# Kernel optimization log

Hardware: AMD Instinct MI355X
Metric: run time of the kernel (lower is better)

Reference implementation:

```python
import jax, jax.numpy as jnp
import numpy as np

B, L, H = 1, 2048, 2048          # batch, seq_len, hidden_size
E, N, K, R = 4096, 16, 4, 128    # intermediate, ssm_state, conv_kernel, dt_rank


def setup_inputs() -> dict:
    key = jax.random.key(0)
    ks = jax.random.split(key, 8)
    s = 0.02
    inp = {
        "hidden_states": jax.random.normal(ks[0], (B, L, H), jnp.float32),
        "in_proj_w": jax.random.normal(ks[1], (2 * E, H), jnp.float32) * s,
        "conv_w": jax.random.normal(ks[2], (E, 1, K), jnp.float32) * s,
        "conv_b": jax.random.normal(ks[3], (E,), jnp.float32) * s,
        "x_proj_w": jax.random.normal(ks[4], (R + 2 * N, E), jnp.float32) * s,
        "dt_proj_w": jax.random.normal(ks[5], (E, R), jnp.float32) * s,
        "dt_proj_b": jax.random.normal(ks[6], (E,), jnp.float32) * s,
        "A_log": jnp.broadcast_to(jnp.log(jnp.arange(1, N + 1, dtype=jnp.float32))[None, :], (E, N)).copy(),
        "D": jnp.ones((E,), jnp.float32),
        "out_proj_w": jax.random.normal(ks[7], (H, E), jnp.float32) * s,
    }
    return inp


def _mamba_mixer(hidden_states, in_proj_w, conv_w, conv_b, x_proj_w,
                 dt_proj_w, dt_proj_b, A_log, D, out_proj_w):
    # in_proj -> [B, L, 2E], split into hidden / gate
    proj = jnp.einsum('blh,eh->ble', hidden_states, in_proj_w)
    h, gate = jnp.split(proj, 2, axis=-1)            # each [B, L, E]

    # depthwise causal conv1d over time, padding K-1 on the left
    h_c = h.transpose(0, 2, 1)                       # [B, E, L]
    h_c = jax.lax.conv_general_dilated(
        h_c, conv_w, window_strides=(1,), padding=[(K - 1, 0)],
        feature_group_count=E, dimension_numbers=('NCH', 'OIH', 'NCH'))
    h_c = h_c + conv_b[None, :, None]
    h = jax.nn.silu(h_c).transpose(0, 2, 1)          # [B, L, E]

    # x_proj -> dt, B, C (input-dependent SSM params)
    ssm = jnp.einsum('ble,pe->blp', h, x_proj_w)     # [B, L, R+2N]
    dt, Bp, Cp = jnp.split(ssm, [R, R + N], axis=-1)
    dt = jax.nn.softplus(jnp.einsum('blr,er->ble', dt, dt_proj_w) + dt_proj_b)  # [B,L,E]

    A = -jnp.exp(A_log)                              # [E, N]
    dA = jnp.exp(dt[..., None] * A)                  # [B, L, E, N]
    dBu = (dt * h)[..., None] * Bp[:, :, None, :]    # [B, L, E, N]

    # selective scan: s_t = dA_t * s_{t-1} + dBu_t
    def step(s, xs):
        dA_t, dBu_t = xs
        s = s * dA_t + dBu_t
        return s, s

    s0 = jnp.zeros((h.shape[0], E, N), h.dtype)
    _, states = jax.lax.scan(step, s0, (dA.transpose(1, 0, 2, 3), dBu.transpose(1, 0, 2, 3)))
    # states: [L, B, E, N]
    y = jnp.einsum('lben,bln->ble', states, Cp)      # [B, L, E]
    y = y + h * D                                    # skip via D
    y = y * jax.nn.silu(gate)                        # gated output
    return jnp.einsum('ble,he->blh', y, out_proj_w)  # [B, L, H]


def reference(hidden_states, in_proj_w, conv_w, conv_b, x_proj_w,
              dt_proj_w, dt_proj_b, A_log, D, out_proj_w):
    return _mamba_mixer(hidden_states, in_proj_w, conv_w, conv_b, x_proj_w,
                        dt_proj_w, dt_proj_b, A_log, D, out_proj_w)
```

## Files before the change

### kernel.cpp

```cpp
#include <hip/hip_runtime.h>

#define LL 2048
#define HH 2048
#define EE 4096
#define NS 16
#define RR 128
#define CT 32
#define NC (LL / CT)
#define BM 128
#define BN 128
#define BK 64

typedef __bf16 bf16x8 __attribute__((ext_vector_type(8)));
typedef float f32x4 __attribute__((ext_vector_type(4)));

__device__ __forceinline__ unsigned short f2bf(float f) {
  union { float f; unsigned int u; } v; v.f = f;
  unsigned int r = v.u + 0x7fffu + ((v.u >> 16) & 1u);
  return (unsigned short)(r >> 16);
}

__device__ __forceinline__ float bf2f(unsigned short u) {
  union { unsigned int i; float f; } v;
  v.i = ((unsigned int)u) << 16;
  return v.f;
}

__device__ __forceinline__ float softplus_fast(float x) {
  if (x > 20.0f) return x;
  float e = __builtin_amdgcn_exp2f(1.44269504f * x);
  return 0.69314718f * __builtin_amdgcn_logf(1.0f + e);
}

__device__ __forceinline__ void async_cp16(const unsigned short* g,
                                           unsigned short* l) {
  __builtin_amdgcn_global_load_lds(
      (const __attribute__((address_space(1))) unsigned int*)g,
      (__attribute__((address_space(3))) unsigned int*)l, 16, 0, 0);
}

__global__ void cast_bf16_k(const float* __restrict__ in,
                            unsigned short* __restrict__ out, int n4) {
  int i = blockIdx.x * blockDim.x + threadIdx.x;
  if (i >= n4) return;
  float4 v = reinterpret_cast<const float4*>(in)[i];
  ushort4 o;
  o.x = f2bf(v.x); o.y = f2bf(v.y); o.z = f2bf(v.z); o.w = f2bf(v.w);
  reinterpret_cast<ushort4*>(out)[i] = o;
}

__global__ void zero_k(float* __restrict__ p, int n4) {
  int i = blockIdx.x * blockDim.x + threadIdx.x;
  if (i >= n4) return;
  float4 z; z.x = z.y = z.z = z.w = 0.0f;
  reinterpret_cast<float4*>(p)[i] = z;
}

template <int EPI>
__global__ __launch_bounds__(512, 2) void gemm256(
    const unsigned short* __restrict__ A,
    const unsigned short* __restrict__ B,
    float* __restrict__ C,
    int M, int N, int K, int tilesM, int splitk,
    float* __restrict__ auxF, unsigned short* __restrict__ auxB) {
  __shared__ __align__(16) unsigned short As[2][16384];
  __shared__ __align__(16) unsigned short Bs[2][16384];

  int bid = blockIdx.x;
  int tnInner = bid & 7;
  int rest = bid >> 3;
  int tm = rest % tilesM;
  int tn = (rest / tilesM) * 8 + tnInner;

  int Kslice = K / splitk;
  int k_begin = blockIdx.y * Kslice;
  int NT = Kslice / 64;

  int tid = threadIdx.x;
  int lane = tid & 63;
  int wave = tid >> 6;
  int wm = wave >> 2;
  int wn = wave & 3;
  int m16 = lane & 15, quad = lane >> 4;

  const unsigned short* Ab = A + (size_t)tm * 256 * K;
  const unsigned short* Bb = B + (size_t)tn * 256 * K;

  int rowS = tid >> 3;
  int gcbS = (tid & 7) ^ (rowS & 7);
  int ldsWB = (tid & ~63) * 8;

  int sw = m16 & 7;
  int coff0 = (quad ^ sw) << 3;
  int coff1 = ((4 + quad) ^ sw) << 3;
  int aoff = (wm * 128 + m16) * 64;
  int boff = (wn * 64 + m16) * 64;

  f32x4 acc[8][4];
#pragma unroll
  for (int i = 0; i < 8; ++i)
#pragma unroll
    for (int j = 0; j < 4; ++j)
#pragma unroll
      for (int t = 0; t < 4; ++t) acc[i][j][t] = 0.0f;

  auto stageA = [&](int bufb, int t, int h) {
    int kt = k_begin + t * 64;
    unsigned short* dst = &As[bufb][0];
#pragma unroll
    for (int c = 2 * h; c < 2 * h + 2; ++c)
      async_cp16(Ab + (size_t)(c * 64 + rowS) * K + kt + gcbS * 8,
                 dst + c * 4096 + ldsWB);
  };
  auto stageB = [&](int bufb, int t, int h) {
    int kt = k_begin + t * 64;
    unsigned short* dst = &Bs[bufb][0];
#pragma unroll
    for (int c = 2 * h; c < 2 * h + 2; ++c)
      async_cp16(Bb + (size_t)(c * 64 + rowS) * K + kt + gcbS * 8,
                 dst + c * 4096 + ldsWB);
  };

  stageA(0, 0, 0); stageA(0, 0, 1);
  stageB(0, 0, 0); stageB(0, 0, 1);
  stageB(1, 1, 0); stageB(1, 1, 1);
  stageA(1, 1, 0);
  asm volatile("s_waitcnt vmcnt(6)" ::: "memory");
  __builtin_amdgcn_s_barrier();

  bf16x8 a[4][2], b0[2][2], b1[2][2];

  for (int t0 = 0; t0 < NT; t0 += 2) {
    int t1 = t0 + 1;
    bool notLast = (t0 + 2 < NT);
    unsigned short* A0 = &As[0][0];
    unsigned short* B0 = &Bs[0][0];
    unsigned short* A1 = &As[1][0];
    unsigned short* B1 = &Bs[1][0];

#pragma unroll
    for (int i = 0; i < 4; ++i) {
      a[i][0] = *reinterpret_cast<const bf16x8*>(&A0[aoff + i * 1024 + coff0]);
      a[i][1] = *reinterpret_cast<const bf16x8*>(&A0[aoff + i * 1024 + coff1]);
    }
#pragma unroll
    for (int j = 0; j < 2; ++j) {
      b0[j][0] = *reinterpret_cast<const bf16x8*>(&B0[boff + j * 1024 + coff0]);
      b0[j][1] = *reinterpret_cast<const bf16x8*>(&B0[boff + j * 1024 + coff1]);
    }
    stageA(1, t1, 1);
    __builtin_amdgcn_s_barrier();
    asm volatile("s_waitcnt lgkmcnt(0)" ::: "memory");
    __builtin_amdgcn_sched_barrier(0);
    __builtin_amdgcn_s_setprio(1);
#pragma unroll
    for (int kk = 0; kk < 2; ++kk)
#pragma unroll
      for (int i = 0; i < 4; ++i)
#pragma unroll
        for (int j = 0; j < 2; ++j)
          acc[i][j] = __builtin_amdgcn_mfma_f32_16x16x32_bf16(
              a[i][kk], b0[j][kk], acc[i][j], 0, 0, 0);
    __builtin_amdgcn_s_setprio(0);
    __builtin_amdgcn_s_barrier();

#pragma unroll
    for (int j = 0; j < 2; ++j) {
      b1[j][0] = *reinterpret_cast<const bf16x8*>(&B0[boff + (2 + j) * 1024 + coff0]);
      b1[j][1] = *reinterpret_cast<const bf16x8*>(&B0[boff + (2 + j) * 1024 + coff1]);
    }
    __builtin_amdgcn_s_barrier();
    asm volatile("s_waitcnt lgkmcnt(0)" ::: "memory");
    __builtin_amdgcn_sched_barrier(0);
    __builtin_amdgcn_s_setprio(1);
#pragma unroll
    for (int kk = 0; kk < 2; ++kk)
#pragma unroll
      for (int i = 0; i < 4; ++i)
#pragma unroll
        for (int j = 0; j < 2; ++j)
          acc[i][2 + j] = __builtin_amdgcn_mfma_f32_16x16x32_bf16(
              a[i][kk], b1[j][kk], acc[i][2 + j], 0, 0, 0);
    __builtin_amdgcn_s_setprio(0);
    __builtin_amdgcn_s_barrier();

#pragma unroll
    for (int i = 0; i < 4; ++i) {
      a[i][0] = *reinterpret_cast<const bf16x8*>(&A0[aoff + (4 + i) * 1024 + coff0]);
      a[i][1] = *reinterpret_cast<const bf16x8*>(&A0[aoff + (4 + i) * 1024 + coff1]);
    }
    if (notLast) stageB(0, t0 + 2, 0);
    __builtin_amdgcn_s_barrier();
    asm volatile("s_waitcnt lgkmcnt(0)" ::: "memory");
    __builtin_amdgcn_sched_barrier(0);
    __builtin_amdgcn_s_setprio(1);
#pragma unroll
    for (int kk = 0; kk < 2; ++kk)
#pragma unroll
      for (int i = 0; i < 4; ++i)
#pragma unroll
        for (int j = 0; j < 2; ++j)
          acc[4 + i][2 + j] = __builtin_amdgcn_mfma_f32_16x16x32_bf16(
              a[i][kk], b1[j][kk], acc[4 + i][2 + j], 0, 0, 0);
    __builtin_amdgcn_s_setprio(0);
    __builtin_amdgcn_s_barrier();

    if (notLast) stageB(0, t0 + 2, 1);
    __builtin_amdgcn_s_setprio(1);
#pragma unroll
    for (int kk = 0; kk < 2; ++kk)
#pragma unroll
      for (int i = 0; i < 4; ++i)
#pragma unroll
        for (int j = 0; j < 2; ++j)
          acc[4 + i][j] = __builtin_amdgcn_mfma_f32_16x16x32_bf16(
              a[i][kk], b0[j][kk], acc[4 + i][j], 0, 0, 0);
    __builtin_amdgcn_s_setprio(0);
    if (notLast) {
      asm volatile("s_waitcnt vmcnt(4)" ::: "memory");
    } else {
      asm volatile("s_waitcnt vmcnt(0)" ::: "memory");
    }
    __builtin_amdgcn_s_barrier();

#pragma unroll
    for (int i = 0; i < 4; ++i) {
      a[i][0] = *reinterpret_cast<const bf16x8*>(&A1[aoff + i * 1024 + coff0]);
      a[i][1] = *reinterpret_cast<const bf16x8*>(&A1[aoff + i * 1024 + coff1]);
    }
#pragma unroll
    for (int j = 0; j < 2; ++j) {
      b0[j][0] = *reinterpret_cast<const bf16x8*>(&B1[boff + j * 1024 + coff0]);
      b0[j][1] = *reinterpret_cast<const bf16x8*>(&B1[boff + j * 1024 + coff1]);
    }
    if (notLast) stageA(0, t0 + 2, 0);
    __builtin_amdgcn_s_barrier();
    asm volatile("s_waitcnt lgkmcnt(0)" ::: "memory");
    __builtin_amdgcn_sched_barrier(0);
    __builtin_amdgcn_s_setprio(1);
#pragma unroll
    for (int kk = 0; kk < 2; ++kk)
#pragma unroll
      for (int i = 0; i < 4; ++i)
#pragma unroll
        for (int j = 0; j < 2; ++j)
          acc[i][j] = __builtin_amdgcn_mfma_f32_16x16x32_bf16(
              a[i][kk], b0[j][kk], acc[i][j], 0, 0, 0);
    __builtin_amdgcn_s_setprio(0);
    __builtin_amdgcn_s_barrier();

#pragma unroll
    for (int j = 0; j < 2; ++j) {
      b1[j][0] = *reinterpret_cast<const bf16x8*>(&B1[boff + (2 + j) * 1024 + coff0]);
      b1[j][1] = *reinterpret_cast<const bf16x8*>(&B1[boff + (2 + j) * 1024 + coff1]);
    }
    if (notLast) stageA(0, t0 + 2, 1);
    __builtin_amdgcn_s_barrier();
    asm volatile("s_waitcnt lgkmcnt(0)" ::: "memory");
    __builtin_amdgcn_sched_barrier(0);
    __builtin_amdgcn_s_setprio(1);
#pragma unroll
    for (int kk = 0; kk < 2; ++kk)
#pragma unroll
      for (int i = 0; i < 4; ++i)
#pragma unroll
        for (int j = 0; j < 2; ++j)
          acc[i][2 + j] = __builtin_amdgcn_mfma_f32_16x16x32_bf16(
              a[i][kk], b1[j][kk], acc[i][2 + j], 0, 0, 0);
    __builtin_amdgcn_s_setprio(0);
    __builtin_amdgcn_s_barrier();

#pragma unroll
    for (int i = 0; i < 4; ++i) {
      a[i][0] = *reinterpret_cast<const bf16x8*>(&A1[aoff + (4 + i) * 1024 + coff0]);
      a[i][1] = *reinterpret_cast<const bf16x8*>(&A1[aoff + (4 + i) * 1024 + coff1]);
    }
    if (notLast) stageB(1, t1 + 2, 0);
    __builtin_amdgcn_s_barrier();
    asm volatile("s_waitcnt lgkmcnt(0)" ::: "memory");
    __builtin_amdgcn_sched_barrier(0);
    __builtin_amdgcn_s_setprio(1);
#pragma unroll
    for (int kk = 0; kk < 2; ++kk)
#pragma unroll
      for (int i = 0; i < 4; ++i)
#pragma unroll
        for (int j = 0; j < 2; ++j)
          acc[4 + i][2 + j] = __builtin_amdgcn_mfma_f32_16x16x32_bf16(
              a[i][kk], b1[j][kk], acc[4 + i][2 + j], 0, 0, 0);
    __builtin_amdgcn_s_setprio(0);
    __builtin_amdgcn_s_barrier();

    if (notLast) { stageB(1, t1 + 2, 1); stageA(1, t1 + 2, 0); }
    __builtin_amdgcn_s_setprio(1);
#pragma unroll
    for (int kk = 0; kk < 2; ++kk)
#pragma unroll
      for (int i = 0; i < 4; ++i)
#pragma unroll
        for (int j = 0; j < 2; ++j)
          acc[4 + i][j] = __builtin_amdgcn_mfma_f32_16x16x32_bf16(
              a[i][kk], b0[j][kk], acc[4 + i][j], 0, 0, 0);
    __builtin_amdgcn_s_setprio(0);
    if (notLast) {
      asm volatile("s_waitcnt vmcnt(6)" ::: "memory");
    }
    __builtin_amdgcn_s_barrier();
  }

  int rowB = tm * 256 + wm * 128;
  int colB = tn * 256 + wn * 64;
  if constexpr (EPI == 1) {
#pragma unroll
    for (int mi = 0; mi < 8; ++mi)
#pragma unroll
      for (int nj = 0; nj < 4; ++nj) {
        int col = colB + nj * 16 + m16;
        int row0 = rowB + mi * 16 + quad * 4;
#pragma unroll
        for (int t4 = 0; t4 < 4; ++t4)
          atomicAdd(&C[(size_t)(row0 + t4) * N + col], acc[mi][nj][t4]);
      }
  } else {
    if (colB < EE) {
#pragma unroll
      for (int mi = 0; mi < 8; ++mi)
#pragma unroll
        for (int nj = 0; nj < 4; ++nj) {
          int col = colB + nj * 16 + m16;
          int row0 = rowB + mi * 16 + quad * 4;
#pragma unroll
          for (int t4 = 0; t4 < 4; ++t4)
            auxF[(size_t)(row0 + t4) * EE + col] = acc[mi][nj][t4];
        }
    } else {
#pragma unroll
      for (int mi = 0; mi < 8; ++mi)
#pragma unroll
        for (int nj = 0; nj < 4; ++nj) {
          int cg = colB + nj * 16 + m16 - EE;
          int row0 = rowB + mi * 16 + quad * 4;
#pragma unroll
          for (int t4 = 0; t4 < 4; ++t4) {
            float v = acc[mi][nj][t4];
            float s = v / (1.0f + __expf(-v));
            auxB[(size_t)(row0 + t4) * EE + cg] = f2bf(s);
          }
        }
    }
  }
}

template <int EPI>
__global__ __launch_bounds__(256) void gemm_lds_t(
    const unsigned short* __restrict__ A,
    const unsigned short* __restrict__ B,
    float* __restrict__ C,
    int M, int N, int K, int tilesM, int splitk,
    const float* __restrict__ bias, float* __restrict__ auxF,
    unsigned short* __restrict__ auxB) {
  __shared__ __align__(16) unsigned short As[BM * BK];
  __shared__ __align__(16) unsigned short Bs[BN * BK];

  int bid = blockIdx.x;
  int tnInner = bid & 7;
  int rest = bid >> 3;
  int tm = rest % tilesM;
  int tnOuter = rest / tilesM;
  int tn = tnOuter * 8 + tnInner;

  int Kslice = K / splitk;
  int k_begin = blockIdx.y * Kslice;
  int k_end = k_begin + Kslice;

  int tid = threadIdx.x;
  int lane = tid & 63;
  int wave = tid >> 6;
  int wm = wave & 1, wn = wave >> 1;
  int m16 = lane & 15, quad = lane >> 4;

  const unsigned short* Ab = A + (size_t)tm * BM * K;
  const unsigned short* Bb = B + (size_t)tn * BN * K;

  int srow[4], sgcb[4];
#pragma unroll
  for (int it = 0; it < 4; ++it) {
    int blk = it * 256 + tid;
    srow[it] = blk >> 3;
    sgcb[it] = (blk & 7) ^ (srow[it] & 7);
  }
  int ldsbase = (tid & ~63) * 8;

  f32x4 acc[4][4];
#pragma unroll
  for (int i = 0; i < 4; ++i)
#pragma unroll
    for (int j = 0; j < 4; ++j)
#pragma unroll
      for (int t = 0; t < 4; ++t) acc[i][j][t] = 0.0f;

  for (int k0 = k_begin; k0 < k_end; k0 += BK) {
    __syncthreads();
#pragma unroll
    for (int it = 0; it < 4; ++it)
      async_cp16(Ab + (size_t)srow[it] * K + k0 + sgcb[it] * 8,
                 &As[it * 2048 + ldsbase]);
#pragma unroll
    for (int it = 0; it < 4; ++it)
      async_cp16(Bb + (size_t)srow[it] * K + k0 + sgcb[it] * 8,
                 &Bs[it * 2048 + ldsbase]);
    __syncthreads();
#pragma unroll
    for (int kk = 0; kk < 2; ++kk) {
      bf16x8 a[4], b[4];
#pragma unroll
      for (int i = 0; i < 4; ++i) {
        int rr = wm * 64 + i * 16 + m16;
        int cb = (kk << 2) + quad;
        a[i] = *reinterpret_cast<const bf16x8*>(
            &As[rr * BK + ((cb ^ (rr & 7)) << 3)]);
      }
#pragma unroll
      for (int j = 0; j < 4; ++j) {
        int rr = wn * 64 + j * 16 + m16;
        int cb = (kk << 2) + quad;
        b[j] = *reinterpret_cast<const bf16x8*>(
            &Bs[rr * BK + ((cb ^ (rr & 7)) << 3)]);
      }
#pragma unroll
      for (int i = 0; i < 4; ++i)
#pragma unroll
        for (int j = 0; j < 4; ++j)
          acc[i][j] =
              __builtin_amdgcn_mfma_f32_16x16x32_bf16(a[i], b[j], acc[i][j], 0, 0, 0);
    }
  }

  int rowB = tm * BM + wm * 64;
  int colB = tn * BN + wn * 64;
  if constexpr (EPI == 1) {
#pragma unroll
    for (int i = 0; i < 4; ++i)
#pragma unroll
      for (int j = 0; j < 4; ++j) {
        int col = colB + j * 16 + m16;
        int row0 = rowB + i * 16 + quad * 4;
#pragma unroll
        for (int t = 0; t < 4; ++t)
          atomicAdd(&C[(size_t)(row0 + t) * N + col], acc[i][j][t]);
      }
  } else {
#pragma unroll
    for (int i = 0; i < 4; ++i)
#pragma unroll
      for (int j = 0; j < 4; ++j) {
        int col = colB + j * 16 + m16;
        float bv = bias[col];
        int row0 = rowB + i * 16 + quad * 4;
#pragma unroll
        for (int t = 0; t < 4; ++t) {
          float x = acc[i][j][t] + bv;
          auxB[(size_t)(row0 + t) * EE + col] = f2bf(softplus_fast(x));
        }
      }
  }
}

__global__ __launch_bounds__(256) void gemm_bt(
    const unsigned short* __restrict__ A,
    const unsigned short* __restrict__ B,
    float* __restrict__ C,
    int M, int N, int K, int tilesN, int splitk) {
  int bid = blockIdx.x;
  int groupSize = 8 * tilesN;
  int g = bid / groupSize, r = bid % groupSize;
  int tm = g * 8 + (r & 7);
  int tn = r >> 3;

  int Kslice = K / splitk;
  int k_begin = blockIdx.y * Kslice;
  int k_end = k_begin + Kslice;

  int tid = threadIdx.x;
  int wave = tid >> 6, lane = tid & 63;
  int wm = wave & 1, wn = wave >> 1;
  int m16 = lane & 15, quad = lane >> 4;
  int rowBase = tm * 64 + wm * 32;
  int colBase = tn * 128 + wn * 64;

  const unsigned short* a0p = A + (size_t)(rowBase + m16) * K + quad * 8;
  const unsigned short* a1p = A + (size_t)(rowBase + 16 + m16) * K + quad * 8;
  const unsigned short* bp[4];
  bool bok[4];
#pragma unroll
  for (int j = 0; j < 4; ++j) {
    int col = colBase + j * 16 + m16;
    bok[j] = (col < N);
    bp[j] = B + (size_t)(bok[j] ? col : 0) * K + quad * 8;
  }

  f32x4 acc[2][4];
#pragma unroll
  for (int i = 0; i < 2; ++i)
#pragma unroll
    for (int j = 0; j < 4; ++j)
#pragma unroll
      for (int t = 0; t < 4; ++t) acc[i][j][t] = 0.0f;

  bf16x8 zero8;
#pragma unroll
  for (int t = 0; t < 8; ++t) zero8[t] = (__bf16)0.0f;

  for (int k = k_begin; k < k_end; k += 32) {
    bf16x8 a0 = *reinterpret_cast<const bf16x8*>(a0p + k);
    bf16x8 a1 = *reinterpret_cast<const bf16x8*>(a1p + k);
    bf16x8 b[4];
#pragma unroll
    for (int j = 0; j < 4; ++j)
      b[j] = bok[j] ? *reinterpret_cast<const bf16x8*>(bp[j] + k) : zero8;
#pragma unroll
    for (int j = 0; j < 4; ++j) {
      acc[0][j] = __builtin_amdgcn_mfma_f32_16x16x32_bf16(a0, b[j], acc[0][j], 0, 0, 0);
      acc[1][j] = __builtin_amdgcn_mfma_f32_16x16x32_bf16(a1, b[j], acc[1][j], 0, 0, 0);
    }
  }

#pragma unroll
  for (int i = 0; i < 2; ++i)
#pragma unroll
    for (int j = 0; j < 4; ++j) {
      int col = colBase + j * 16 + m16;
      if (col >= N) continue;
      int row0 = rowBase + i * 16 + quad * 4;
      if (splitk == 1) {
#pragma unroll
        for (int t = 0; t < 4; ++t)
          C[(size_t)(row0 + t) * N + col] = acc[i][j][t];
      } else {
#pragma unroll
        for (int t = 0; t < 4; ++t)
          atomicAdd(&C[(size_t)(row0 + t) * N + col], acc[i][j][t]);
      }
    }
}

__global__ __launch_bounds__(256) void conv_silu_k(
    const float* __restrict__ projh, const float* __restrict__ cw,
    const float* __restrict__ cb, unsigned short* __restrict__ hb) {
  int e = blockIdx.x * 256 + threadIdx.x;
  int l0 = blockIdx.y * 16;
  float w0 = cw[e * 4 + 0], w1 = cw[e * 4 + 1];
  float w2 = cw[e * 4 + 2], w3 = cw[e * 4 + 3];
  float bias = cb[e];
  float xm3 = (l0 >= 3) ? projh[(size_t)(l0 - 3) * EE + e] : 0.0f;
  float xm2 = (l0 >= 2) ? projh[(size_t)(l0 - 2) * EE + e] : 0.0f;
  float xm1 = (l0 >= 1) ? projh[(size_t)(l0 - 1) * EE + e] : 0.0f;
#pragma unroll
  for (int t = 0; t < 16; ++t) {
    int l = l0 + t;
    float x0 = projh[(size_t)l * EE + e];
    float acc = bias + w0 * xm3 + w1 * xm2 + w2 * xm1 + w3 * x0;
    float s = acc / (1.0f + __expf(-acc));
    hb[(size_t)l * EE + e] = f2bf(s);
    xm3 = xm2; xm2 = xm1; xm1 = x0;
  }
}

__global__ void dtcast_k(const float* __restrict__ ssm,
                         unsigned short* __restrict__ dtin, int n) {
  int i = blockIdx.x * blockDim.x + threadIdx.x;
  if (i >= n) return;
  int l = i >> 7, r = i & 127;
  dtin[i] = f2bf(ssm[l * 160 + r]);
}

__global__ __launch_bounds__(256) void scan_partA(
    const unsigned short* __restrict__ dtb, const unsigned short* __restrict__ hb,
    const float* __restrict__ ssm, const float* __restrict__ A_log,
    float* __restrict__ P, float* __restrict__ S) {
  int e = blockIdx.y * 256 + threadIdx.x;
  int c = blockIdx.x;
  float Aa[16];
#pragma unroll
  for (int q = 0; q < 4; ++q) {
    float4 a = reinterpret_cast<const float4*>(&A_log[(size_t)e * NS])[q];
    Aa[q * 4 + 0] = -__expf(a.x) * 1.44269504f;
    Aa[q * 4 + 1] = -__expf(a.y) * 1.44269504f;
    Aa[q * 4 + 2] = -__expf(a.z) * 1.44269504f;
    Aa[q * 4 + 3] = -__expf(a.w) * 1.44269504f;
  }
  float s[16], p[16];
#pragma unroll
  for (int n = 0; n < 16; ++n) { s[n] = 0.0f; p[n] = 1.0f; }
  int l0 = c * CT;
#pragma unroll 2
  for (int t = 0; t < CT; ++t) {
    int l = l0 + t;
    size_t o = (size_t)l * EE + e;
    float dtv = bf2f(dtb[o]);
    float hv = bf2f(hb[o]);
    float Bv[16];
#pragma unroll
    for (int q = 0; q < 4; ++q)
      *reinterpret_cast<float4*>(&Bv[q * 4]) =
          reinterpret_cast<const float4*>(&ssm[(size_t)l * 160 + 128])[q];
    float z = dtv * hv;
#pragma unroll
    for (int n = 0; n < 16; ++n) {
      float dA = __builtin_amdgcn_exp2f(dtv * Aa[n]);
      s[n] = s[n] * dA + z * Bv[n];
      p[n] *= dA;
    }
  }
  size_t base = ((size_t)c * EE + e) * NS;
#pragma unroll
  for (int q = 0; q < 4; ++q) {
    reinterpret_cast<float4*>(&P[base])[q] = *reinterpret_cast<float4*>(&p[q * 4]);
    reinterpret_cast<float4*>(&S[base])[q] = *reinterpret_cast<float4*>(&s[q * 4]);
  }
}

__global__ __launch_bounds__(256) void scan_chunkB(
    const float* __restrict__ P, float* __restrict__ S) {
  int gidx = blockIdx.x * 256 + threadIdx.x;
  float s = 0.0f;
  float pv = P[gidx], sv = S[gidx];
  for (int c = 0; c < NC; ++c) {
    float pn = 0.0f, sn = 0.0f;
    if (c + 1 < NC) {
      size_t i2 = (size_t)(c + 1) * (EE * NS) + gidx;
      pn = P[i2];
      sn = S[i2];
    }
    float s_next = s * pv + sv;
    S[(size_t)c * (EE * NS) + gidx] = s;
    s = s_next;
    pv = pn; sv = sn;
  }
}

__global__ __launch_bounds__(256) void scan_partC(
    const unsigned short* __restrict__ dtb, const unsigned short* __restrict__ hb,
    const float* __restrict__ ssm, const float* __restrict__ A_log,
    const float* __restrict__ Dp, const unsigned short* __restrict__ sg,
    const float* __restrict__ Sinit, unsigned short* __restrict__ yb) {
  int e = blockIdx.y * 256 + threadIdx.x;
  int c = blockIdx.x;
  float Aa[16];
#pragma unroll
  for (int q = 0; q < 4; ++q) {
    float4 a = reinterpret_cast<const float4*>(&A_log[(size_t)e * NS])[q];
    Aa[q * 4 + 0] = -__expf(a.x) * 1.44269504f;
    Aa[q * 4 + 1] = -__expf(a.y) * 1.44269504f;
    Aa[q * 4 + 2] = -__expf(a.z) * 1.44269504f;
    Aa[q * 4 + 3] = -__expf(a.w) * 1.44269504f;
  }
  float Dv = Dp[e];
  float s[16];
  size_t base = ((size_t)c * EE + e) * NS;
#pragma unroll
  for (int q = 0; q < 4; ++q)
    *reinterpret_cast<float4*>(&s[q * 4]) =
        reinterpret_cast<const float4*>(&Sinit[base])[q];
  int l0 = c * CT;
#pragma unroll 2
  for (int t = 0; t < CT; ++t) {
    int l = l0 + t;
    size_t o = (size_t)l * EE + e;
    float dtv = bf2f(dtb[o]);
    float hv = bf2f(hb[o]);
    float Bv[16], Cv[16];
#pragma unroll
    for (int q = 0; q < 4; ++q) {
      *reinterpret_cast<float4*>(&Bv[q * 4]) =
          reinterpret_cast<const float4*>(&ssm[(size_t)l * 160 + 128])[q];
      *reinterpret_cast<float4*>(&Cv[q * 4]) =
          reinterpret_cast<const float4*>(&ssm[(size_t)l * 160 + 144])[q];
    }
    float z = dtv * hv;
    float y = 0.0f;
#pragma unroll
    for (int n = 0; n < 16; ++n) {
      float dA = __builtin_amdgcn_exp2f(dtv * Aa[n]);
      s[n] = s[n] * dA + z * Bv[n];
      y += s[n] * Cv[n];
    }
    float gv = bf2f(sg[o]);
    float yv = (y + hv * Dv) * gv;
    yb[o] = f2bf(yv);
  }
}

extern "C" void kernel_launch(void* const* d_in, const int* in_sizes, int n_in,
                              void* d_out, int out_size, void* d_ws, size_t ws_size,
                              hipStream_t stream) {
  const float* hs   = (const float*)d_in[0];
  const float* w1   = (const float*)d_in[1];
  const float* cw   = (const float*)d_in[2];
  const float* cb   = (const float*)d_in[3];
  const float* xw   = (const float*)d_in[4];
  const float* dtw  = (const float*)d_in[5];
  const float* dtb  = (const float*)d_in[6];
  const float* Alog = (const float*)d_in[7];
  const float* Dp   = (const float*)d_in[8];
  const float* ow   = (const float*)d_in[9];
  float* out = (float*)d_out;

  char* ws = (char*)d_ws;
  size_t off = 0;
  auto alloc = [&](size_t b) {
    char* p = ws + off;
    off += (b + 255) & ~(size_t)255;
    return p;
  };
  float* projh = (float*)alloc((size_t)LL * EE * 4);
  unsigned short* sg  = (unsigned short*)alloc((size_t)LL * EE * 2);
  unsigned short* hb  = (unsigned short*)alloc((size_t)LL * EE * 2);
  unsigned short* dtb_buf = (unsigned short*)alloc((size_t)LL * EE * 2);
  unsigned short* w1b = (unsigned short*)alloc((size_t)2 * EE * HH * 2);
  unsigned short* hsb = (unsigned short*)alloc((size_t)LL * HH * 2);
  unsigned short* yb  = (unsigned short*)alloc((size_t)LL * EE * 2);
  unsigned short* owb = (unsigned short*)alloc((size_t)HH * EE * 2);
  unsigned short* xwb = (unsigned short*)alloc((size_t)160 * EE * 2);
  float* ssm = (float*)alloc((size_t)LL * 160 * 4);
  unsigned short* dtin = (unsigned short*)alloc((size_t)LL * RR * 2);
  unsigned short* dtwb = (unsigned short*)alloc((size_t)EE * RR * 2);
  float* Pbuf = (float*)alloc((size_t)NC * EE * NS * 4);
  float* Sbuf = (float*)alloc((size_t)NC * EE * NS * 4);

  auto cast = [&](const float* in, unsigned short* o, int nelem) {
    int n4 = nelem / 4;
    cast_bf16_k<<<(n4 + 255) / 256, 256, 0, stream>>>(in, o, n4);
  };
  cast(hs, hsb, LL * HH);
  cast(w1, w1b, 2 * EE * HH);
  cast(xw, xwb, 160 * EE);
  cast(dtw, dtwb, EE * RR);
  cast(ow, owb, HH * EE);
  zero_k<<<(LL * 160 / 4 + 255) / 256, 256, 0, stream>>>(ssm, LL * 160 / 4);
  zero_k<<<(LL * HH / 4 + 255) / 256, 256, 0, stream>>>(out, LL * HH / 4);

  {
    int tilesM = LL / 256;
    int tilesN = (2 * EE) / 256;
    gemm256<2><<<dim3(tilesM * tilesN, 1), 512, 0, stream>>>(
        hsb, w1b, nullptr, LL, 2 * EE, HH, tilesM, 1, projh, sg);
  }
  conv_silu_k<<<dim3(EE / 256, LL / 16), 256, 0, stream>>>(projh, cw, cb, hb);
  {
    int tilesN = (160 + 127) / 128, tilesM = LL / 64;
    gemm_bt<<<dim3(tilesM * tilesN, 8), 256, 0, stream>>>(
        hb, xwb, ssm, LL, 160, EE, tilesN, 8);
  }
  dtcast_k<<<(LL * RR + 255) / 256, 256, 0, stream>>>(ssm, dtin, LL * RR);
  {
    int tilesN = EE / BN, tilesM = LL / BM;
    gemm_lds_t<4><<<dim3(tilesM * tilesN, 1), 256, 0, stream>>>(
        dtin, dtwb, nullptr, LL, EE, RR, tilesM, 1, dtb, nullptr, dtb_buf);
  }
  scan_partA<<<dim3(NC, EE / 256), 256, 0, stream>>>(dtb_buf, hb, ssm, Alog,
                                                     Pbuf, Sbuf);
  scan_chunkB<<<EE * NS / 256, 256, 0, stream>>>(Pbuf, Sbuf);
  scan_partC<<<dim3(NC, EE / 256), 256, 0, stream>>>(dtb_buf, hb, ssm, Alog, Dp,
                                                     sg, Sbuf, yb);
  {
    int tilesN = HH / BN, tilesM = LL / BM;
    gemm_lds_t<1><<<dim3(tilesM * tilesN, 2), 256, 0, stream>>>(
        yb, owb, out, LL, HH, EE, tilesM, 2, nullptr, nullptr, nullptr);
  }
}
```

Measured before the change: 419.6 us.

## Fuse cast/zero launches into one prep kernel; use 256-tile GEMM for out_proj

The five bf16 cast launches and two zero-fill launches are merged into a single prep kernel that picks its source and destination by index range, cutting launch overhead. The output projection moves from the 128x128 LDS GEMM with split-K 2 to the 256x256, 512-thread GEMM with split-K 4. The larger tile gives more data reuse per block. The cost is more atomic split-K accumulation into the output and only 64 tiles times 4 splits of parallelism.

```diff
diff --git a/kernel.cpp b/kernel.cpp
--- a/kernel.cpp
+++ b/kernel.cpp
@@ -39,21 +39,43 @@
       (__attribute__((address_space(3))) unsigned int*)l, 16, 0, 0);
 }
 
-__global__ void cast_bf16_k(const float* __restrict__ in,
-                            unsigned short* __restrict__ out, int n4) {
-  int i = blockIdx.x * blockDim.x + threadIdx.x;
-  if (i >= n4) return;
-  float4 v = reinterpret_cast<const float4*>(in)[i];
+#define P_C0 (LL * HH / 4)
+#define P_C1 (P_C0 + 2 * EE * HH / 4)
+#define P_C2 (P_C1 + 160 * EE / 4)
+#define P_C3 (P_C2 + EE * RR / 4)
+#define P_C4 (P_C3 + HH * EE / 4)
+#define P_C5 (P_C4 + LL * 160 / 4)
+#define P_C6 (P_C5 + LL * HH / 4)
+
+__global__ __launch_bounds__(256) void prep_k(
+    const float* __restrict__ hs, unsigned short* __restrict__ hsb,
+    const float* __restrict__ w1, unsigned short* __restrict__ w1b,
+    const float* __restrict__ xw, unsigned short* __restrict__ xwb,
+    const float* __restrict__ dtw, unsigned short* __restrict__ dtwb,
+    const float* __restrict__ ow, unsigned short* __restrict__ owb,
+    float* __restrict__ ssm, float* __restrict__ out) {
+  int i = blockIdx.x * 256 + threadIdx.x;
+  const float* src = nullptr;
+  unsigned short* dst = nullptr;
+  int k = 0;
+  if (i < P_C0)      { src = hs;  dst = hsb;  k = i; }
+  else if (i < P_C1) { src = w1;  dst = w1b;  k = i - P_C0; }
+  else if (i < P_C2) { src = xw;  dst = xwb;  k = i - P_C1; }
+  else if (i < P_C3) { src = dtw; dst = dtwb; k = i - P_C2; }
+  else if (i < P_C4) { src = ow;  dst = owb;  k = i - P_C3; }
+  else if (i < P_C5) {
+    float4 z; z.x = z.y = z.z = z.w = 0.0f;
+    reinterpret_cast<float4*>(ssm)[i - P_C4] = z;
+    return;
+  } else {
+    float4 z; z.x = z.y = z.z = z.w = 0.0f;
+    reinterpret_cast<float4*>(out)[i - P_C5] = z;
+    return;
+  }
+  float4 v = reinterpret_cast<const float4*>(src)[k];
   ushort4 o;
   o.x = f2bf(v.x); o.y = f2bf(v.y); o.z = f2bf(v.z); o.w = f2bf(v.w);
-  reinterpret_cast<ushort4*>(out)[i] = o;
-}
-
-__global__ void zero_k(float* __restrict__ p, int n4) {
-  int i = blockIdx.x * blockDim.x + threadIdx.x;
-  if (i >= n4) return;
-  float4 z; z.x = z.y = z.z = z.w = 0.0f;
-  reinterpret_cast<float4*>(p)[i] = z;
+  reinterpret_cast<ushort4*>(dst)[k] = o;
 }
 
 template <int EPI>
@@ -728,17 +750,8 @@
   float* Pbuf = (float*)alloc((size_t)NC * EE * NS * 4);
   float* Sbuf = (float*)alloc((size_t)NC * EE * NS * 4);
 
-  auto cast = [&](const float* in, unsigned short* o, int nelem) {
-    int n4 = nelem / 4;
-    cast_bf16_k<<<(n4 + 255) / 256, 256, 0, stream>>>(in, o, n4);
-  };
-  cast(hs, hsb, LL * HH);
-  cast(w1, w1b, 2 * EE * HH);
-  cast(xw, xwb, 160 * EE);
-  cast(dtw, dtwb, EE * RR);
-  cast(ow, owb, HH * EE);
-  zero_k<<<(LL * 160 / 4 + 255) / 256, 256, 0, stream>>>(ssm, LL * 160 / 4);
-  zero_k<<<(LL * HH / 4 + 255) / 256, 256, 0, stream>>>(out, LL * HH / 4);
+  prep_k<<<P_C6 / 256, 256, 0, stream>>>(hs, hsb, w1, w1b, xw, xwb, dtw, dtwb,
+                                         ow, owb, ssm, out);
 
   {
     int tilesM = LL / 256;
@@ -764,8 +777,8 @@
   scan_partC<<<dim3(NC, EE / 256), 256, 0, stream>>>(dtb_buf, hb, ssm, Alog, Dp,
                                                      sg, Sbuf, yb);
   {
-    int tilesN = HH / BN, tilesM = LL / BM;
-    gemm_lds_t<1><<<dim3(tilesM * tilesN, 2), 256, 0, stream>>>(
-        yb, owb, out, LL, HH, EE, tilesM, 2, nullptr, nullptr, nullptr);
-  }
-}
+    int tilesM = LL / 256, tilesN = HH / 256;
+    gemm256<1><<<dim3(tilesM * tilesN, 4), 512, 0, stream>>>(
+        yb, owb, out, LL, HH, EE, tilesM, 4, nullptr, nullptr);
+  }
+}
```

New measurement: 435.5 us. 1.04x slower.
